# Performance work log

Hardware: AMD Instinct MI355X
Metric: run time of the kernel (lower is better)

Reference implementation:

```python
import jax, jax.numpy as jnp
import numpy as np

B, T, FEA = 8, 4096, 512      # input: fea = 2*IN_C real values
IN_C = FEA // 2               # complex input units
H_C = 256                     # complex hidden units (hidden_size init arg)
NUM_LAYERS = 2


def _clin(x, wr, wi, br, bi):
    """Complex linear: x=[..., 2*in] (real half then imag half) -> [..., 2*out]."""
    xr, xi = jnp.split(x, 2, axis=-1)
    yr = xr @ wr - xi @ wi + br
    yi = xr @ wi + xi @ wr + bi
    return jnp.concatenate([yr, yi], axis=-1)


def _rnn_layer(x, wr, wi, wbr, wbi, ur, ui, ubr, ubi):
    # x: [B, T, 2*in_c] -> h: [B, T, 2*H_C]
    wx = _clin(x, wr, wi, wbr, wbi)          # [B, T, 2*H_C] (input proj, one big GEMM)
    wx_t = jnp.swapaxes(wx, 0, 1)            # [T, B, 2*H_C] for scan over time
    h0 = jnp.zeros((x.shape[0], 2 * H_C), dtype=x.dtype)  # h_init = zeros

    def step(h, wt):
        h_new = jnp.tanh(wt + _clin(h, ur, ui, ubr, ubi))  # act(w_t + U h); eval drop_mask=1
        return h_new, h_new

    _, hs = jax.lax.scan(step, h0, wx_t)     # [T, B, 2*H_C]
    return jnp.swapaxes(hs, 0, 1)            # [B, T, 2*H_C]


def setup_inputs() -> dict:
    key = jax.random.key(0)
    ks = jax.random.split(key, 1 + 8 * NUM_LAYERS)
    inp = {"x": jax.random.normal(ks[0], (B, T, FEA), dtype=jnp.float32)}
    in_c = IN_C
    ki = 1
    for l in range(NUM_LAYERS):
        sw = 1.0 / np.sqrt(2.0 * in_c)   # glorot-ish scale for input proj
        su = 1.0 / np.sqrt(2.0 * H_C)    # recurrent weight scale (keeps tanh unsaturated)
        inp[f"l{l}_wr"] = jax.random.normal(ks[ki + 0], (in_c, H_C), jnp.float32) * sw
        inp[f"l{l}_wi"] = jax.random.normal(ks[ki + 1], (in_c, H_C), jnp.float32) * sw
        inp[f"l{l}_wbr"] = jnp.zeros((H_C,), jnp.float32)
        inp[f"l{l}_wbi"] = jnp.zeros((H_C,), jnp.float32)
        inp[f"l{l}_ur"] = jax.random.normal(ks[ki + 2], (H_C, H_C), jnp.float32) * su
        inp[f"l{l}_ui"] = jax.random.normal(ks[ki + 3], (H_C, H_C), jnp.float32) * su
        inp[f"l{l}_ubr"] = jnp.zeros((H_C,), jnp.float32)
        inp[f"l{l}_ubi"] = jnp.zeros((H_C,), jnp.float32)
        ki += 4
        in_c = H_C  # next layer consumes 2*H_C real values -> H_C complex
    return inp


def reference(x,
              l0_wr, l0_wi, l0_wbr, l0_wbi, l0_ur, l0_ui, l0_ubr, l0_ubi,
              l1_wr, l1_wi, l1_wbr, l1_wbi, l1_ur, l1_ui, l1_ubr, l1_ubi):
    h = _rnn_layer(x, l0_wr, l0_wi, l0_wbr, l0_wbi, l0_ur, l0_ui, l0_ubr, l0_ubi)
    h = _rnn_layer(h, l1_wr, l1_wi, l1_wbr, l1_wbi, l1_ur, l1_ui, l1_ubr, l1_ubi)
    return h  # [B, T, 2*H_C]
```

## Files before the change

kernel.cpp:

```cpp
#include <hip/hip_runtime.h>

typedef unsigned int uint;
typedef unsigned long long u64;
typedef __attribute__((ext_vector_type(4))) float f32x4;
typedef __attribute__((ext_vector_type(8))) short s16x8;

union U4 { uint u[4]; s16x8 v; uint4 q; };

#define TT 4096
#define HC2 512
#define SENT 0xFFFFFFFFu

__device__ __forceinline__ uint bf16_rne(float f) {
  uint x = __float_as_uint(f);
  x += 0x7fffu + ((x >> 16) & 1u);
  return x >> 16;
}
__device__ __forceinline__ uint pack_split(float f) {
  uint hi = bf16_rne(f);
  float fh = __uint_as_float(hi << 16);
  uint lo = bf16_rne(f - fh);
  return hi | (lo << 16);
}
__device__ __forceinline__ float unpack_split(uint w) {
  return __uint_as_float(w << 16) + __uint_as_float(w & 0xffff0000u);
}
__device__ __forceinline__ float fast_tanh(float y) {
  float e = __builtin_amdgcn_exp2f(y * 2.885390081777927f);
  return 1.0f - 2.0f * __builtin_amdgcn_rcpf(e + 1.0f);
}

__device__ __forceinline__ void st_sys(uint* p, uint v) {
  asm volatile("global_store_dword %0, %1, off sc0 sc1" :: "v"(p), "v"(v) : "memory");
}
__device__ __forceinline__ void ld16_sys(const uint* p, uint4& a, uint4& b, uint4& c, uint4& d) {
  asm volatile("global_load_dwordx4 %0, %4, off sc0 sc1\n\t"
               "global_load_dwordx4 %1, %4, off offset:16 sc0 sc1\n\t"
               "global_load_dwordx4 %2, %4, off offset:32 sc0 sc1\n\t"
               "global_load_dwordx4 %3, %4, off offset:48 sc0 sc1\n\t"
               "s_waitcnt vmcnt(0)"
               : "=&v"(a), "=&v"(b), "=&v"(c), "=&v"(d) : "v"(p) : "memory");
}
__device__ __forceinline__ void ld16z_sys(const uint* p, const uint* zp,
                                          uint4& a, uint4& b, uint4& c, uint4& d,
                                          uint& z0, uint& z1, uint& z2, uint& z3) {
  asm volatile("global_load_dwordx4 %0, %8, off sc0 sc1\n\t"
               "global_load_dwordx4 %1, %8, off offset:16 sc0 sc1\n\t"
               "global_load_dwordx4 %2, %8, off offset:32 sc0 sc1\n\t"
               "global_load_dwordx4 %3, %8, off offset:48 sc0 sc1\n\t"
               "global_load_dword %4, %9, off sc0 sc1\n\t"
               "global_load_dword %5, %9, off offset:256 sc0 sc1\n\t"
               "global_load_dword %6, %9, off offset:512 sc0 sc1\n\t"
               "global_load_dword %7, %9, off offset:768 sc0 sc1\n\t"
               "s_waitcnt vmcnt(0)"
               : "=&v"(a), "=&v"(b), "=&v"(c), "=&v"(d),
                 "=&v"(z0), "=&v"(z1), "=&v"(z2), "=&v"(z3)
               : "v"(p), "v"(zp) : "memory");
}
__device__ __forceinline__ void ld4z_sys(const uint* zp, uint& z0, uint& z1, uint& z2, uint& z3) {
  asm volatile("global_load_dword %0, %4, off sc0 sc1\n\t"
               "global_load_dword %1, %4, off offset:256 sc0 sc1\n\t"
               "global_load_dword %2, %4, off offset:512 sc0 sc1\n\t"
               "global_load_dword %3, %4, off offset:768 sc0 sc1\n\t"
               "s_waitcnt vmcnt(0)"
               : "=&v"(z0), "=&v"(z1), "=&v"(z2), "=&v"(z3) : "v"(zp) : "memory");
}

__global__ void pack_weights_kernel(const float* __restrict__ wr, const float* __restrict__ wi,
                                    const float* __restrict__ wbr, const float* __restrict__ wbi,
                                    const float* __restrict__ ur, const float* __restrict__ ui,
                                    const float* __restrict__ ubr, const float* __restrict__ ubi,
                                    uint* __restrict__ MwT, uint* __restrict__ MuT,
                                    float* __restrict__ bias) {
  const int id = blockIdx.x * 256 + threadIdx.x;
  const int j = id >> 9, k = id & 511;
  const int jj = j & 255, kk = k & 255;
  float mw, mu;
  if (k < 256) {
    if (j < 256) { mw =  wr[kk * 256 + jj]; mu =  ur[kk * 256 + jj]; }
    else         { mw =  wi[kk * 256 + jj]; mu =  ui[kk * 256 + jj]; }
  } else {
    if (j < 256) { mw = -wi[kk * 256 + jj]; mu = -ui[kk * 256 + jj]; }
    else         { mw =  wr[kk * 256 + jj]; mu =  ur[kk * 256 + jj]; }
  }
  MwT[id] = pack_split(mw);
  MuT[id] = pack_split(mu);
  if (id < 512)
    bias[id] = (id < 256) ? (wbr[id] + ubr[id]) : (wbi[id - 256] + ubi[id - 256]);
}

__global__ void pack_x_kernel(const float* __restrict__ x, uint* __restrict__ xp) {
  const u64 i = ((u64)blockIdx.x * 256 + threadIdx.x) * 4;
  float4 v = *(const float4*)(x + i);
  uint4 o;
  o.x = pack_split(v.x); o.y = pack_split(v.y);
  o.z = pack_split(v.z); o.w = pack_split(v.w);
  *(uint4*)(xp + i) = o;
}

__global__ __launch_bounds__(256, 2)
void gemm_split_kernel(const uint* __restrict__ A, const uint* __restrict__ BT,
                       const float* __restrict__ bias, float* __restrict__ C) {
  __shared__ __align__(16) uint a_s[128][36];
  __shared__ __align__(16) uint b_s[128][36];
  const int tid = threadIdx.x;
  const int wv = tid >> 6, lane = tid & 63;
  const int q = lane >> 4, cl = lane & 15;
  const int row0 = (int)blockIdx.x * 128, col0 = (int)blockIdx.y * 128;
  const int wro = (wv >> 1) * 64, wco = (wv & 1) * 64;
  const int sr = tid >> 1, sc = (tid & 1) * 16;

  f32x4 acc[4][4];
#pragma unroll
  for (int a = 0; a < 4; ++a)
#pragma unroll
    for (int b = 0; b < 4; ++b) acc[a][b] = (f32x4){0.f, 0.f, 0.f, 0.f};

  const uint* ga = A + (u64)(row0 + sr) * 512 + sc;
  const uint* gb = BT + (u64)(col0 + sr) * 512 + sc;

  for (int kb = 0; kb < 16; ++kb) {
    uint4 va0 = *(const uint4*)(ga + 0), va1 = *(const uint4*)(ga + 4);
    uint4 va2 = *(const uint4*)(ga + 8), va3 = *(const uint4*)(ga + 12);
    uint4 vb0 = *(const uint4*)(gb + 0), vb1 = *(const uint4*)(gb + 4);
    uint4 vb2 = *(const uint4*)(gb + 8), vb3 = *(const uint4*)(gb + 12);
    ga += 32; gb += 32;
    __syncthreads();
    *(uint4*)&a_s[sr][sc + 0] = va0;  *(uint4*)&a_s[sr][sc + 4] = va1;
    *(uint4*)&a_s[sr][sc + 8] = va2;  *(uint4*)&a_s[sr][sc + 12] = va3;
    *(uint4*)&b_s[sr][sc + 0] = vb0;  *(uint4*)&b_s[sr][sc + 4] = vb1;
    *(uint4*)&b_s[sr][sc + 8] = vb2;  *(uint4*)&b_s[sr][sc + 12] = vb3;
    __syncthreads();

    s16x8 ah[4], al[4];
#pragma unroll
    for (int rt = 0; rt < 4; ++rt) {
      const uint* p = &a_s[wro + rt * 16 + cl][q * 8];
      uint4 p0 = *(const uint4*)(p), p1 = *(const uint4*)(p + 4);
      U4 th, tl;
      th.u[0] = (p0.x & 0xffffu) | (p0.y << 16);
      th.u[1] = (p0.z & 0xffffu) | (p0.w << 16);
      th.u[2] = (p1.x & 0xffffu) | (p1.y << 16);
      th.u[3] = (p1.z & 0xffffu) | (p1.w << 16);
      tl.u[0] = (p0.x >> 16) | (p0.y & 0xffff0000u);
      tl.u[1] = (p0.z >> 16) | (p0.w & 0xffff0000u);
      tl.u[2] = (p1.x >> 16) | (p1.y & 0xffff0000u);
      tl.u[3] = (p1.z >> 16) | (p1.w & 0xffff0000u);
      ah[rt] = th.v; al[rt] = tl.v;
    }
#pragma unroll
    for (int ct = 0; ct < 4; ++ct) {
      const uint* p = &b_s[wco + ct * 16 + cl][q * 8];
      uint4 p0 = *(const uint4*)(p), p1 = *(const uint4*)(p + 4);
      U4 th, tl;
      th.u[0] = (p0.x & 0xffffu) | (p0.y << 16);
      th.u[1] = (p0.z & 0xffffu) | (p0.w << 16);
      th.u[2] = (p1.x & 0xffffu) | (p1.y << 16);
      th.u[3] = (p1.z & 0xffffu) | (p1.w << 16);
      tl.u[0] = (p0.x >> 16) | (p0.y & 0xffff0000u);
      tl.u[1] = (p0.z >> 16) | (p0.w & 0xffff0000u);
      tl.u[2] = (p1.x >> 16) | (p1.y & 0xffff0000u);
      tl.u[3] = (p1.z >> 16) | (p1.w & 0xffff0000u);
#pragma unroll
      for (int rt = 0; rt < 4; ++rt) {
        acc[rt][ct] = __builtin_amdgcn_mfma_f32_16x16x32_bf16(ah[rt], th.v, acc[rt][ct], 0, 0, 0);
        acc[rt][ct] = __builtin_amdgcn_mfma_f32_16x16x32_bf16(al[rt], th.v, acc[rt][ct], 0, 0, 0);
        acc[rt][ct] = __builtin_amdgcn_mfma_f32_16x16x32_bf16(ah[rt], tl.v, acc[rt][ct], 0, 0, 0);
      }
    }
  }
#pragma unroll
  for (int ct = 0; ct < 4; ++ct) {
    const int col = col0 + wco + ct * 16 + cl;
    const float bv = bias[col];
#pragma unroll
    for (int rt = 0; rt < 4; ++rt) {
      const int rbase = row0 + wro + rt * 16 + q * 4;
#pragma unroll
      for (int r2 = 0; r2 < 4; ++r2)
        C[(u64)(rbase + r2) * 512 + col] = acc[rt][ct][r2] + bv;
    }
  }
}

__global__ __launch_bounds__(256, 1)
void fused_scan_kernel(const uint* __restrict__ MuT0, const float* __restrict__ wxb,
                       const uint* __restrict__ MwT1, const uint* __restrict__ MuT1,
                       const float* __restrict__ bias1,
                       uint* __restrict__ xpk0,
                       uint* __restrict__ h1x,
                       uint* __restrict__ zbuf) {
  __shared__ __align__(16) unsigned short xah[16][520];
  __shared__ __align__(16) unsigned short xal[16][520];
  const int tid = threadIdx.x;
  const int wv = tid >> 6, lane = tid & 63;
  const int q = lane >> 4, cl = lane & 15;
  const int role = (int)blockIdx.x >> 3;
  const int blk = (int)blockIdx.x & 7;
  const int j = blk * 64 + wv * 16 + cl;
  const int jc = wv * 16 + cl;

  for (int idx = tid; idx < 16 * 520; idx += 256) {
    ((unsigned short*)xah)[idx] = 0; ((unsigned short*)xal)[idx] = 0;
  }

  uint4 bh4[16], bl4[16];
  {
    const uint* wsel = (role == 0) ? MuT0 : ((role == 1) ? MwT1 : MuT1);
    const uint* wrow = wsel + (u64)j * 512;
#pragma unroll
    for (int ks = 0; ks < 16; ++ks) {
      const int k0 = ks * 32 + q * 8;
      uint4 p0 = *(const uint4*)(wrow + k0);
      uint4 p1 = *(const uint4*)(wrow + k0 + 4);
      uint4 h, l;
      h.x = (p0.x & 0xffffu) | (p0.y << 16);
      h.y = (p0.z & 0xffffu) | (p0.w << 16);
      h.z = (p1.x & 0xffffu) | (p1.y << 16);
      h.w = (p1.z & 0xffffu) | (p1.w << 16);
      l.x = (p0.x >> 16) | (p0.y & 0xffff0000u);
      l.y = (p0.z >> 16) | (p0.w & 0xffff0000u);
      l.z = (p1.x >> 16) | (p1.y & 0xffff0000u);
      l.w = (p1.z >> 16) | (p1.w & 0xffff0000u);
      bh4[ks] = h; bl4[ks] = l;
    }
  }
  __syncthreads();

  const int srow = tid >> 5;
  const int scol = (tid & 31) * 16;
  bool timeout = false;

  if (role == 0) {
    const uint* hsrc_base = xpk0 + (u64)srow * TT * HC2 + scol;
#pragma unroll 1
    for (int t = 0; t < TT; ++t) {
      float wpre[4] = {0.f, 0.f, 0.f, 0.f};
      if (q < 2) {
#pragma unroll
        for (int r = 0; r < 4; ++r)
          wpre[r] = wxb[((u64)(q * 4 + r) * TT + t) * HC2 + j];
      }
      f32x4 acc0 = {0.f, 0.f, 0.f, 0.f}, acc1 = acc0, acc2 = acc0;
      if (t > 0) {
        const uint* src = hsrc_base + (u64)(t - 1) * HC2;
        uint4 p0, p1, p2, p3;
        int spin = 0;
        for (;;) {
          ld16_sys(src, p0, p1, p2, p3);
          bool ok = timeout ||
                    (p0.x != SENT && p0.y != SENT && p0.z != SENT && p0.w != SENT &&
                     p1.x != SENT && p1.y != SENT && p1.z != SENT && p1.w != SENT &&
                     p2.x != SENT && p2.y != SENT && p2.z != SENT && p2.w != SENT &&
                     p3.x != SENT && p3.y != SENT && p3.z != SENT && p3.w != SENT);
          if (__ballot(ok) == ~0ull) break;
          if (++spin > (1 << 20)) { timeout = true; break; }
          __builtin_amdgcn_s_sleep(1);
        }
        {
          uint pcs[16] = {p0.x, p0.y, p0.z, p0.w, p1.x, p1.y, p1.z, p1.w,
                          p2.x, p2.y, p2.z, p2.w, p3.x, p3.y, p3.z, p3.w};
          U4 h0, h1, l0, l1;
#pragma unroll
          for (int e = 0; e < 4; ++e) {
            h0.u[e] = (pcs[2 * e] & 0xffffu) | (pcs[2 * e + 1] << 16);
            l0.u[e] = (pcs[2 * e] >> 16) | (pcs[2 * e + 1] & 0xffff0000u);
            h1.u[e] = (pcs[8 + 2 * e] & 0xffffu) | (pcs[8 + 2 * e + 1] << 16);
            l1.u[e] = (pcs[8 + 2 * e] >> 16) | (pcs[8 + 2 * e + 1] & 0xffff0000u);
          }
          *(uint4*)&xah[srow][scol] = h0.q;  *(uint4*)&xah[srow][scol + 8] = h1.q;
          *(uint4*)&xal[srow][scol] = l0.q;  *(uint4*)&xal[srow][scol + 8] = l1.q;
        }
        __syncthreads();
#pragma unroll
        for (int ks = 0; ks < 16; ++ks) {
          const int k0 = ks * 32 + q * 8;
          s16x8 ah = *(const s16x8*)&xah[cl][k0];
          s16x8 al = *(const s16x8*)&xal[cl][k0];
          U4 tb, tc; tb.q = bh4[ks]; tc.q = bl4[ks];
          acc0 = __builtin_amdgcn_mfma_f32_16x16x32_bf16(ah, tb.v, acc0, 0, 0, 0);
          acc1 = __builtin_amdgcn_mfma_f32_16x16x32_bf16(al, tb.v, acc1, 0, 0, 0);
          acc2 = __builtin_amdgcn_mfma_f32_16x16x32_bf16(ah, tc.v, acc2, 0, 0, 0);
        }
      }
      if (q < 2) {
#pragma unroll
        for (int r = 0; r < 4; ++r) {
          const int b = q * 4 + r;
          const u64 off = ((u64)b * TT + t) * HC2 + j;
          float y = acc0[r] + acc1[r] + acc2[r] + wpre[r];
          st_sys(xpk0 + off, pack_split(fast_tanh(y)));
        }
      }
    }
  } else if (role == 1) {
    const uint* h0src_base = xpk0 + (u64)srow * TT * HC2 + scol;
    const float bv = bias1[j];
#pragma unroll 1
    for (int t = 0; t < TT; ++t) {
      const uint* src = h0src_base + (u64)t * HC2;
      uint4 p0, p1, p2, p3;
      int spin = 0;
      for (;;) {
        ld16_sys(src, p0, p1, p2, p3);
        bool ok = timeout ||
                  (p0.x != SENT && p0.y != SENT && p0.z != SENT && p0.w != SENT &&
                   p1.x != SENT && p1.y != SENT && p1.z != SENT && p1.w != SENT &&
                   p2.x != SENT && p2.y != SENT && p2.z != SENT && p2.w != SENT &&
                   p3.x != SENT && p3.y != SENT && p3.z != SENT && p3.w != SENT);
        if (__ballot(ok) == ~0ull) break;
        if (++spin > (1 << 20)) { timeout = true; break; }
        __builtin_amdgcn_s_sleep(1);
      }
      {
        uint pcs[16] = {p0.x, p0.y, p0.z, p0.w, p1.x, p1.y, p1.z, p1.w,
                        p2.x, p2.y, p2.z, p2.w, p3.x, p3.y, p3.z, p3.w};
        U4 h0, h1, l0, l1;
#pragma unroll
        for (int e = 0; e < 4; ++e) {
          h0.u[e] = (pcs[2 * e] & 0xffffu) | (pcs[2 * e + 1] << 16);
          l0.u[e] = (pcs[2 * e] >> 16) | (pcs[2 * e + 1] & 0xffff0000u);
          h1.u[e] = (pcs[8 + 2 * e] & 0xffffu) | (pcs[8 + 2 * e + 1] << 16);
          l1.u[e] = (pcs[8 + 2 * e] >> 16) | (pcs[8 + 2 * e + 1] & 0xffff0000u);
        }
        *(uint4*)&xah[srow][scol] = h0.q;  *(uint4*)&xah[srow][scol + 8] = h1.q;
        *(uint4*)&xal[srow][scol] = l0.q;  *(uint4*)&xal[srow][scol + 8] = l1.q;
      }
      __syncthreads();
      f32x4 a0 = {0.f, 0.f, 0.f, 0.f}, a1 = a0, a2 = a0;
#pragma unroll
      for (int ks = 0; ks < 16; ++ks) {
        const int k0 = ks * 32 + q * 8;
        s16x8 yh = *(const s16x8*)&xah[cl][k0];
        s16x8 yl = *(const s16x8*)&xal[cl][k0];
        U4 tb, tc; tb.q = bh4[ks]; tc.q = bl4[ks];
        a0 = __builtin_amdgcn_mfma_f32_16x16x32_bf16(yh, tb.v, a0, 0, 0, 0);
        a1 = __builtin_amdgcn_mfma_f32_16x16x32_bf16(yl, tb.v, a1, 0, 0, 0);
        a2 = __builtin_amdgcn_mfma_f32_16x16x32_bf16(yh, tc.v, a2, 0, 0, 0);
      }
      if (q < 2) {
        uint* zo = zbuf + (((u64)blk * TT + t) * 8 + q * 4) * 64 + jc;
#pragma unroll
        for (int r = 0; r < 4; ++r) {
          float z = a0[r] + a1[r] + a2[r] + bv;
          st_sys(zo + r * 64, pack_split(z));
        }
      }
      __syncthreads();
    }
  } else {
    const uint* h1src_base = h1x + (u64)srow * TT * HC2 + scol;
#pragma unroll 1
    for (int t = 0; t < TT; ++t) {
      const uint* zp = zbuf + ((q < 2) ? ((((u64)blk * TT + t) * 8 + q * 4) * 64 + jc) : 0);
      uint zw0, zw1, zw2, zw3;
      int spin = 0;
      if (t == 0) {
        for (;;) {
          ld4z_sys(zp, zw0, zw1, zw2, zw3);
          bool ok = timeout || q >= 2 ||
                    (zw0 != SENT && zw1 != SENT && zw2 != SENT && zw3 != SENT);
          if (__ballot(ok) == ~0ull) break;
          if (++spin > (1 << 20)) { timeout = true; break; }
          __builtin_amdgcn_s_sleep(1);
        }
        __syncthreads();
      } else {
        const uint* src = h1src_base + (u64)(t - 1) * HC2;
        uint4 p0, p1, p2, p3;
        for (;;) {
          ld16z_sys(src, zp, p0, p1, p2, p3, zw0, zw1, zw2, zw3);
          bool ok = timeout ||
                    ((p0.x != SENT && p0.y != SENT && p0.z != SENT && p0.w != SENT &&
                      p1.x != SENT && p1.y != SENT && p1.z != SENT && p1.w != SENT &&
                      p2.x != SENT && p2.y != SENT && p2.z != SENT && p2.w != SENT &&
                      p3.x != SENT && p3.y != SENT && p3.z != SENT && p3.w != SENT) &&
                     (q >= 2 ||
                      (zw0 != SENT && zw1 != SENT && zw2 != SENT && zw3 != SENT)));
          if (__ballot(ok) == ~0ull) break;
          if (++spin > (1 << 20)) { timeout = true; break; }
          __builtin_amdgcn_s_sleep(1);
        }
        {
          uint pf[16] = {p0.x, p0.y, p0.z, p0.w, p1.x, p1.y, p1.z, p1.w,
                         p2.x, p2.y, p2.z, p2.w, p3.x, p3.y, p3.z, p3.w};
          U4 H0, H1, L0, L1;
#pragma unroll
          for (int e = 0; e < 4; ++e) {
            float fa = __uint_as_float(pf[2 * e]);
            float fb = __uint_as_float(pf[2 * e + 1]);
            uint ha = bf16_rne(fa), hb = bf16_rne(fb);
            uint la = bf16_rne(fa - __uint_as_float(ha << 16));
            uint lb = bf16_rne(fb - __uint_as_float(hb << 16));
            H0.u[e] = ha | (hb << 16);
            L0.u[e] = la | (lb << 16);
            float fc = __uint_as_float(pf[8 + 2 * e]);
            float fd = __uint_as_float(pf[8 + 2 * e + 1]);
            uint hc = bf16_rne(fc), hd = bf16_rne(fd);
            uint lc = bf16_rne(fc - __uint_as_float(hc << 16));
            uint ld = bf16_rne(fd - __uint_as_float(hd << 16));
            H1.u[e] = hc | (hd << 16);
            L1.u[e] = lc | (ld << 16);
          }
          *(uint4*)&xah[srow][scol] = H0.q;  *(uint4*)&xah[srow][scol + 8] = H1.q;
          *(uint4*)&xal[srow][scol] = L0.q;  *(uint4*)&xal[srow][scol + 8] = L1.q;
        }
        __syncthreads();
      }
      f32x4 a0 = {0.f, 0.f, 0.f, 0.f}, a1 = a0, a2 = a0;
      if (t > 0) {
#pragma unroll
        for (int ks = 0; ks < 16; ++ks) {
          const int k0 = ks * 32 + q * 8;
          s16x8 ah = *(const s16x8*)&xah[cl][k0];
          s16x8 al = *(const s16x8*)&xal[cl][k0];
          U4 tb, tc; tb.q = bh4[ks]; tc.q = bl4[ks];
          a0 = __builtin_amdgcn_mfma_f32_16x16x32_bf16(ah, tb.v, a0, 0, 0, 0);
          a1 = __builtin_amdgcn_mfma_f32_16x16x32_bf16(al, tb.v, a1, 0, 0, 0);
          a2 = __builtin_amdgcn_mfma_f32_16x16x32_bf16(ah, tc.v, a2, 0, 0, 0);
        }
      }
      if (q < 2) {
        uint zw[4] = {zw0, zw1, zw2, zw3};
#pragma unroll
        for (int r = 0; r < 4; ++r) {
          const int b = q * 4 + r;
          const u64 off = ((u64)b * TT + t) * HC2 + j;
          float y = a0[r] + a1[r] + a2[r] + unpack_split(zw[r]);
          st_sys(h1x + off, __float_as_uint(fast_tanh(y)));
        }
      }
    }
  }
}

extern "C" void kernel_launch(void* const* d_in, const int* in_sizes, int n_in,
                              void* d_out, int out_size, void* d_ws, size_t ws_size,
                              hipStream_t stream) {
  const float* x = (const float*)d_in[0];
  const float* L0[8]; const float* L1[8];
  for (int i = 0; i < 8; ++i) { L0[i] = (const float*)d_in[1 + i]; L1[i] = (const float*)d_in[9 + i]; }

  char* ws = (char*)d_ws;
  const size_t MB = 1024 * 1024;
  uint* MwT0 = (uint*)(ws + 0 * MB);
  uint* MuT0 = (uint*)(ws + 1 * MB);
  uint* MwT1 = (uint*)(ws + 2 * MB);
  uint* MuT1 = (uint*)(ws + 3 * MB);
  float* bias0 = (float*)(ws + 4 * MB);
  float* bias1 = (float*)(ws + 4 * MB + 8192);
  uint* Apk = (uint*)(ws + 8 * MB);
  float* wx = (float*)(ws + 72 * MB);
  uint* zbuf = (uint*)(ws + 136 * MB);

  pack_weights_kernel<<<1024, 256, 0, stream>>>(L0[0], L0[1], L0[2], L0[3], L0[4], L0[5], L0[6], L0[7],
                                                MwT0, MuT0, bias0);
  pack_weights_kernel<<<1024, 256, 0, stream>>>(L1[0], L1[1], L1[2], L1[3], L1[4], L1[5], L1[6], L1[7],
                                                MwT1, MuT1, bias1);
  pack_x_kernel<<<16384, 256, 0, stream>>>(x, Apk);
  gemm_split_kernel<<<dim3(256, 4), 256, 0, stream>>>(Apk, MwT0, bias0, wx);
  hipMemsetAsync(Apk, 0xFF, 64 * MB, stream);
  hipMemsetAsync(d_out, 0xFF, 64 * MB, stream);
  hipMemsetAsync(zbuf, 0xFF, 64 * MB, stream);
  fused_scan_kernel<<<24, 256, 0, stream>>>(MuT0, wx, MwT1, MuT1, bias1, Apk, (uint*)d_out, zbuf);
}
```

Baseline: 12.05 ms.

## Stripe packed hidden-state buffers by 16-column groups along time

Reorders the packed x and layer-0 hidden buffer into [batch][group of 16 columns][time][16], so each consumer thread's per-step 64-byte poll reads a contiguous block that advances along time. Adds an optional separate striped, pre-split bf16 buffer for layer-1 hidden state, so the layer-1 recurrent role no longer re-splits fp32 values after polling. The fp32 output is still written with a plain store. The intent is to cut the cost of cross-block polling and conversion in the serial scan, at the price of strided GEMM A-loads and an extra store per step. The new path depends on the workspace size being at least 264 MB.

```diff
diff --git a/kernel.cpp b/kernel.cpp
--- a/kernel.cpp
+++ b/kernel.cpp
@@ -28,6 +28,10 @@
 __device__ __forceinline__ float fast_tanh(float y) {
   float e = __builtin_amdgcn_exp2f(y * 2.885390081777927f);
   return 1.0f - 2.0f * __builtin_amdgcn_rcpf(e + 1.0f);
+}
+
+__device__ __forceinline__ u64 xoff(int b, int t, int g) {
+  return ((u64)(b * 32 + g) * TT + (u64)t) * 16;
 }
 
 __device__ __forceinline__ void st_sys(uint* p, uint v) {
@@ -90,12 +94,15 @@
 }
 
 __global__ void pack_x_kernel(const float* __restrict__ x, uint* __restrict__ xp) {
-  const u64 i = ((u64)blockIdx.x * 256 + threadIdx.x) * 4;
-  float4 v = *(const float4*)(x + i);
+  const u64 w0 = ((u64)blockIdx.x * 256 + threadIdx.x) * 4;
+  const int b = (int)(w0 >> 21);
+  const int t = (int)((w0 >> 9) & (TT - 1));
+  const int j = (int)(w0 & 511);
+  float4 v = *(const float4*)(x + w0);
   uint4 o;
   o.x = pack_split(v.x); o.y = pack_split(v.y);
   o.z = pack_split(v.z); o.w = pack_split(v.w);
-  *(uint4*)(xp + i) = o;
+  *(uint4*)(xp + xoff(b, t, j >> 4) + (j & 15)) = o;
 }
 
 __global__ __launch_bounds__(256, 2)
@@ -116,15 +123,19 @@
 #pragma unroll
     for (int b = 0; b < 4; ++b) acc[a][b] = (f32x4){0.f, 0.f, 0.f, 0.f};
 
-  const uint* ga = A + (u64)(row0 + sr) * 512 + sc;
+  const int arow = row0 + sr;
+  const int ab = arow >> 12, at = arow & (TT - 1);
+  u64 abase = xoff(ab, at, sc >> 4);
   const uint* gb = BT + (u64)(col0 + sr) * 512 + sc;
 
   for (int kb = 0; kb < 16; ++kb) {
+    const uint* ga = A + abase;
     uint4 va0 = *(const uint4*)(ga + 0), va1 = *(const uint4*)(ga + 4);
     uint4 va2 = *(const uint4*)(ga + 8), va3 = *(const uint4*)(ga + 12);
     uint4 vb0 = *(const uint4*)(gb + 0), vb1 = *(const uint4*)(gb + 4);
     uint4 vb2 = *(const uint4*)(gb + 8), vb3 = *(const uint4*)(gb + 12);
-    ga += 32; gb += 32;
+    abase += (u64)2 * TT * 16;
+    gb += 32;
     __syncthreads();
     *(uint4*)&a_s[sr][sc + 0] = va0;  *(uint4*)&a_s[sr][sc + 4] = va1;
     *(uint4*)&a_s[sr][sc + 8] = va2;  *(uint4*)&a_s[sr][sc + 12] = va3;
@@ -189,6 +200,7 @@
                        const float* __restrict__ bias1,
                        uint* __restrict__ xpk0,
                        uint* __restrict__ h1x,
+                       uint* __restrict__ h1pk,
                        uint* __restrict__ zbuf) {
   __shared__ __align__(16) unsigned short xah[16][520];
   __shared__ __align__(16) unsigned short xal[16][520];
@@ -228,11 +240,13 @@
   __syncthreads();
 
   const int srow = tid >> 5;
-  const int scol = (tid & 31) * 16;
+  const int g = tid & 31;
+  const int scol = g * 16;
+  const uint* x0base = xpk0 + (u64)(srow * 32 + g) * TT * 16;
   bool timeout = false;
 
   if (role == 0) {
-    const uint* hsrc_base = xpk0 + (u64)srow * TT * HC2 + scol;
+    uint* pub = xpk0 + ((u64)((q * 4) * 32 + blk * 4 + wv) * TT * 16) + cl;
 #pragma unroll 1
     for (int t = 0; t < TT; ++t) {
       float wpre[4] = {0.f, 0.f, 0.f, 0.f};
@@ -243,7 +257,7 @@
       }
       f32x4 acc0 = {0.f, 0.f, 0.f, 0.f}, acc1 = acc0, acc2 = acc0;
       if (t > 0) {
-        const uint* src = hsrc_base + (u64)(t - 1) * HC2;
+        const uint* src = x0base + (u64)(t - 1) * 16;
         uint4 p0, p1, p2, p3;
         int spin = 0;
         for (;;) {
@@ -286,19 +300,16 @@
       if (q < 2) {
 #pragma unroll
         for (int r = 0; r < 4; ++r) {
-          const int b = q * 4 + r;
-          const u64 off = ((u64)b * TT + t) * HC2 + j;
           float y = acc0[r] + acc1[r] + acc2[r] + wpre[r];
-          st_sys(xpk0 + off, pack_split(fast_tanh(y)));
+          st_sys(pub + (u64)r * 32 * TT * 16 + (u64)t * 16, pack_split(fast_tanh(y)));
         }
       }
     }
   } else if (role == 1) {
-    const uint* h0src_base = xpk0 + (u64)srow * TT * HC2 + scol;
     const float bv = bias1[j];
 #pragma unroll 1
     for (int t = 0; t < TT; ++t) {
-      const uint* src = h0src_base + (u64)t * HC2;
+      const uint* src = x0base + (u64)t * 16;
       uint4 p0, p1, p2, p3;
       int spin = 0;
       for (;;) {
@@ -349,7 +360,10 @@
       __syncthreads();
     }
   } else {
-    const uint* h1src_base = h1x + (u64)srow * TT * HC2 + scol;
+    const bool hp = (h1pk != nullptr);
+    const uint* h1base_s = hp ? (h1pk + (u64)(srow * 32 + g) * TT * 16) : nullptr;
+    const uint* h1base_c = h1x + (u64)srow * TT * HC2 + scol;
+    uint* pub_s = hp ? (h1pk + ((u64)((q * 4) * 32 + blk * 4 + wv) * TT * 16) + cl) : nullptr;
 #pragma unroll 1
     for (int t = 0; t < TT; ++t) {
       const uint* zp = zbuf + ((q < 2) ? ((((u64)blk * TT + t) * 8 + q * 4) * 64 + jc) : 0);
@@ -366,7 +380,8 @@
         }
         __syncthreads();
       } else {
-        const uint* src = h1src_base + (u64)(t - 1) * HC2;
+        const uint* src = hp ? (h1base_s + (u64)(t - 1) * 16)
+                             : (h1base_c + (u64)(t - 1) * HC2);
         uint4 p0, p1, p2, p3;
         for (;;) {
           ld16z_sys(src, zp, p0, p1, p2, p3, zw0, zw1, zw2, zw3);
@@ -381,7 +396,20 @@
           if (++spin > (1 << 20)) { timeout = true; break; }
           __builtin_amdgcn_s_sleep(1);
         }
-        {
+        if (hp) {
+          uint pcs[16] = {p0.x, p0.y, p0.z, p0.w, p1.x, p1.y, p1.z, p1.w,
+                          p2.x, p2.y, p2.z, p2.w, p3.x, p3.y, p3.z, p3.w};
+          U4 h0, h1, l0, l1;
+#pragma unroll
+          for (int e = 0; e < 4; ++e) {
+            h0.u[e] = (pcs[2 * e] & 0xffffu) | (pcs[2 * e + 1] << 16);
+            l0.u[e] = (pcs[2 * e] >> 16) | (pcs[2 * e + 1] & 0xffff0000u);
+            h1.u[e] = (pcs[8 + 2 * e] & 0xffffu) | (pcs[8 + 2 * e + 1] << 16);
+            l1.u[e] = (pcs[8 + 2 * e] >> 16) | (pcs[8 + 2 * e + 1] & 0xffff0000u);
+          }
+          *(uint4*)&xah[srow][scol] = h0.q;  *(uint4*)&xah[srow][scol + 8] = h1.q;
+          *(uint4*)&xal[srow][scol] = l0.q;  *(uint4*)&xal[srow][scol + 8] = l1.q;
+        } else {
           uint pf[16] = {p0.x, p0.y, p0.z, p0.w, p1.x, p1.y, p1.z, p1.w,
                          p2.x, p2.y, p2.z, p2.w, p3.x, p3.y, p3.z, p3.w};
           U4 H0, H1, L0, L1;
@@ -427,7 +455,13 @@
           const int b = q * 4 + r;
           const u64 off = ((u64)b * TT + t) * HC2 + j;
           float y = a0[r] + a1[r] + a2[r] + unpack_split(zw[r]);
-          st_sys(h1x + off, __float_as_uint(fast_tanh(y)));
+          float h = fast_tanh(y);
+          if (hp) {
+            st_sys(pub_s + (u64)r * 32 * TT * 16 + (u64)t * 16, pack_split(h));
+            h1x[off] = __float_as_uint(h);
+          } else {
+            st_sys(h1x + off, __float_as_uint(h));
+          }
         }
       }
     }
@@ -452,6 +486,8 @@
   uint* Apk = (uint*)(ws + 8 * MB);
   float* wx = (float*)(ws + 72 * MB);
   uint* zbuf = (uint*)(ws + 136 * MB);
+  const bool striped_h1 = ws_size >= (size_t)264 * MB;
+  uint* h1pk = striped_h1 ? (uint*)(ws + 200 * MB) : nullptr;
 
   pack_weights_kernel<<<1024, 256, 0, stream>>>(L0[0], L0[1], L0[2], L0[3], L0[4], L0[5], L0[6], L0[7],
                                                 MwT0, MuT0, bias0);
@@ -460,7 +496,9 @@
   pack_x_kernel<<<16384, 256, 0, stream>>>(x, Apk);
   gemm_split_kernel<<<dim3(256, 4), 256, 0, stream>>>(Apk, MwT0, bias0, wx);
   hipMemsetAsync(Apk, 0xFF, 64 * MB, stream);
-  hipMemsetAsync(d_out, 0xFF, 64 * MB, stream);
   hipMemsetAsync(zbuf, 0xFF, 64 * MB, stream);
-  fused_scan_kernel<<<24, 256, 0, stream>>>(MuT0, wx, MwT1, MuT1, bias1, Apk, (uint*)d_out, zbuf);
-}
+  if (striped_h1) hipMemsetAsync(h1pk, 0xFF, 64 * MB, stream);
+  else            hipMemsetAsync(d_out, 0xFF, 64 * MB, stream);
+  fused_scan_kernel<<<24, 256, 0, stream>>>(MuT0, wx, MwT1, MuT1, bias1, Apk, (uint*)d_out,
+                                            h1pk, zbuf);
+}
```

After: 12.90 ms. 7.1% more time.
